# Performance work log

Measured on AMD Instinct MI355X. Metric: run time of the kernel, lower is better.

Reference implementation:

```python
import jax, jax.numpy as jnp
import numpy as np

N = 100000   # nodes
E = 1600000  # edges
D = 128      # input_dim
H = 128      # hidden_dim
O = 64       # output_dim


def setup_inputs() -> dict:
    key = jax.random.key(0)
    ks = jax.random.split(key, 8)
    x = jax.random.normal(ks[0], (N, D), dtype=jnp.float32)
    edge_index = jax.random.randint(ks[1], (2, E), 0, N, dtype=jnp.int32)
    # Glorot-ish init for weights, zeros for biases (matches GCNConv/Linear defaults in spirit)
    W1 = jax.random.normal(ks[2], (D, H), dtype=jnp.float32) / np.sqrt(D)
    b1 = jnp.zeros((H,), dtype=jnp.float32)
    W2 = jax.random.normal(ks[3], (H, H), dtype=jnp.float32) / np.sqrt(H)
    b2 = jnp.zeros((H,), dtype=jnp.float32)
    Wf = jax.random.normal(ks[4], (H, O), dtype=jnp.float32) / np.sqrt(H)
    bf = jnp.zeros((O,), dtype=jnp.float32)
    return {"x": x, "W1": W1, "b1": b1, "W2": W2, "b2": b2,
            "Wf": Wf, "bf": bf, "edge_index": edge_index}


def gcn_conv(x, W, b, src, dst):
    """GCNConv: out = D^{-1/2} (A + I) D^{-1/2} (x W) + b, edges given as (src->dst)."""
    n = x.shape[0]
    h = x @ W  # [N, H]
    loop = jnp.arange(n, dtype=src.dtype)
    s = jnp.concatenate([src, loop])  # add self-loops
    d = jnp.concatenate([dst, loop])
    deg = jax.ops.segment_sum(jnp.ones_like(s, dtype=h.dtype), d, num_segments=n)
    dinv = jnp.where(deg > 0, jax.lax.rsqrt(deg), 0.0)
    coef = dinv[s] * dinv[d]                              # [E+N]
    msg = h[s] * coef[:, None]                            # gather + scale
    out = jax.ops.segment_sum(msg, d, num_segments=n)     # scatter-add aggregate
    return out + b


def reference(x, W1, b1, W2, b2, Wf, bf, edge_index):
    src, dst = edge_index[0], edge_index[1]
    h = jax.nn.relu(gcn_conv(x, W1, b1, src, dst))
    # dropout is identity in eval mode
    h = jax.nn.relu(gcn_conv(h, W2, b2, src, dst))
    return h @ Wf + bf
```

## Files before the change

kernel.cpp:

```cpp
#include <hip/hip_runtime.h>

#define FD 128
#define SCAN_B 256
#define SCAN_T 256


__global__ void k_deg(const int* __restrict__ dst, int* __restrict__ deg, int E) {
  int e = blockIdx.x * blockDim.x + threadIdx.x;
  if (e < E) atomicAdd(&deg[dst[e]], 1);
}


__global__ __launch_bounds__(SCAN_T) void k_part(const int* __restrict__ deg,
                                                 float* __restrict__ dinv,
                                                 int* __restrict__ part, int n) {
  const int b = blockIdx.x;
  const int chunk = (n + SCAN_B - 1) / SCAN_B;
  const int lo = b * chunk;
  const int hi = min(lo + chunk, n);
  int sum = 0;
  for (int i = lo + threadIdx.x; i < hi; i += SCAN_T) {
    int d = deg[i];
    sum += d;
    dinv[i] = rsqrtf((float)(d + 1));
  }
  __shared__ int red[SCAN_T / 64];
  for (int off = 32; off > 0; off >>= 1) sum += __shfl_down(sum, off, 64);
  if ((threadIdx.x & 63) == 0) red[threadIdx.x >> 6] = sum;
  __syncthreads();
  if (threadIdx.x == 0) {
    int s = 0;
#pragma unroll
    for (int w = 0; w < SCAN_T / 64; ++w) s += red[w];
    part[b] = s;
  }
}

__global__ __launch_bounds__(SCAN_B) void k_scanpart(int* __restrict__ part,
                                                     int* __restrict__ row_ptr, int n) {
  __shared__ int s[SCAN_B];
  const int t = threadIdx.x;
  int v = part[t];
  s[t] = v;
  __syncthreads();
  for (int off = 1; off < SCAN_B; off <<= 1) {
    int u = (t >= off) ? s[t - off] : 0;
    __syncthreads();
    s[t] += u;
    __syncthreads();
  }
  part[t] = s[t] - v;
  if (t == SCAN_B - 1) row_ptr[n] = s[t];
}

__global__ __launch_bounds__(SCAN_T) void k_rowptr(const int* __restrict__ deg,
                                                   const int* __restrict__ part,
                                                   int* __restrict__ row_ptr,
                                                   int* __restrict__ cursor, int n) {
  const int b = blockIdx.x;
  const int chunk = (n + SCAN_B - 1) / SCAN_B;
  const int lo = b * chunk;
  const int hi = min(lo + chunk, n);
  const int sub = (chunk + SCAN_T - 1) / SCAN_T;
  const int t = threadIdx.x;
  const int slo = min(lo + t * sub, hi);
  const int shi = min(slo + sub, hi);
  int sum = 0;
  for (int i = slo; i < shi; ++i) sum += deg[i];
  __shared__ int s[SCAN_T];
  s[t] = sum;
  __syncthreads();
  for (int off = 1; off < SCAN_T; off <<= 1) {
    int u = (t >= off) ? s[t - off] : 0;
    __syncthreads();
    s[t] += u;
    __syncthreads();
  }
  int run = part[b] + s[t] - sum;
  for (int i = slo; i < shi; ++i) {
    row_ptr[i] = run;
    cursor[i]  = run;
    run += deg[i];
  }
}


__global__ void k_fill(const int* __restrict__ src, const int* __restrict__ dst,
                       const float* __restrict__ dinv, int* __restrict__ cursor,
                       int2* __restrict__ csr, int E) {
  int e = blockIdx.x * blockDim.x + threadIdx.x;
  if (e < E) {
    int s = src[e], d = dst[e];
    int pos = atomicAdd(&cursor[d], 1);
    csr[pos] = make_int2(s, __float_as_int(dinv[s] * dinv[d]));
  }
}


__global__ __launch_bounds__(256) void k_gemm(const float* __restrict__ A, int lda,
                                              const float* __restrict__ W, int ldw,
                                              const float* __restrict__ bias,
                                              float* __restrict__ out, int ldo, int nrows) {
  __shared__ float Ws[64 * 64];
  __shared__ float xsT[64 * 128];
  const int t  = threadIdx.x;
  const int c0 = blockIdx.y * 64;
  const int r0 = blockIdx.x * 128;

  const int rgrp = t & 31;
  const int cgrp = t >> 5;

  float acc[4][8];
#pragma unroll
  for (int i = 0; i < 4; ++i)
#pragma unroll
    for (int j = 0; j < 8; ++j)
      acc[i][j] = bias ? bias[c0 + cgrp * 8 + j] : 0.f;

  const int rr = t & 127;
  const int hk = t >> 7;

  for (int half = 0; half < 2; ++half) {
    const int kbase = half * 64;
    __syncthreads();
    for (int i = t; i < 64 * 16; i += 256) {
      int k  = i >> 4;
      int c4 = (i & 15) << 2;
      *reinterpret_cast<float4*>(&Ws[k * 64 + c4]) =
          *reinterpret_cast<const float4*>(&W[(size_t)(kbase + k) * ldw + c0 + c4]);
    }
    {
      const int row = r0 + rr;
      const float* ap = &A[(size_t)row * lda + kbase + hk * 32];
#pragma unroll
      for (int j = 0; j < 8; ++j) {
        float4 v = make_float4(0.f, 0.f, 0.f, 0.f);
        if (row < nrows) v = *reinterpret_cast<const float4*>(ap + j * 4);
        const int kb = hk * 32 + j * 4;
        xsT[(kb + 0) * 128 + rr] = v.x;
        xsT[(kb + 1) * 128 + rr] = v.y;
        xsT[(kb + 2) * 128 + rr] = v.z;
        xsT[(kb + 3) * 128 + rr] = v.w;
      }
    }
    __syncthreads();
#pragma unroll 4
    for (int k = 0; k < 64; ++k) {
      const float4 xv = *reinterpret_cast<const float4*>(&xsT[k * 128 + rgrp * 4]);
      const float4 w0 = *reinterpret_cast<const float4*>(&Ws[k * 64 + cgrp * 8]);
      const float4 w1 = *reinterpret_cast<const float4*>(&Ws[k * 64 + cgrp * 8 + 4]);
      const float x[4] = {xv.x, xv.y, xv.z, xv.w};
      const float w[8] = {w0.x, w0.y, w0.z, w0.w, w1.x, w1.y, w1.z, w1.w};
#pragma unroll
      for (int i = 0; i < 4; ++i)
#pragma unroll
        for (int j = 0; j < 8; ++j)
          acc[i][j] += x[i] * w[j];
    }
  }

#pragma unroll
  for (int i = 0; i < 4; ++i) {
    const int row = r0 + rgrp * 4 + i;
    if (row < nrows) {
      float* o = &out[(size_t)row * ldo + c0 + cgrp * 8];
      *reinterpret_cast<float4*>(o)     = make_float4(acc[i][0], acc[i][1], acc[i][2], acc[i][3]);
      *reinterpret_cast<float4*>(o + 4) = make_float4(acc[i][4], acc[i][5], acc[i][6], acc[i][7]);
    }
  }
}


__global__ __launch_bounds__(256) void k_agg(const float* __restrict__ h,
                                             const int* __restrict__ row_ptr,
                                             const int2* __restrict__ csr,
                                             const float* __restrict__ dinv,
                                             const float* __restrict__ bias,
                                             float* __restrict__ out, int n) {
  const int node = blockIdx.x * 4 + (threadIdx.x >> 6);
  if (node >= n) return;
  const int f2 = (threadIdx.x & 63) << 1;
  const float di = dinv[node];
  float2 hv = *reinterpret_cast<const float2*>(&h[(size_t)node * FD + f2]);
  float accx = hv.x * di * di;
  float accy = hv.y * di * di;
  const int e0 = row_ptr[node], e1 = row_ptr[node + 1];
  int e = e0;
  for (; e + 4 <= e1; e += 4) {
    const int2 E0 = csr[e];
    const int2 E1 = csr[e + 1];
    const int2 E2 = csr[e + 2];
    const int2 E3 = csr[e + 3];
    const float2 v0 = *reinterpret_cast<const float2*>(&h[(size_t)E0.x * FD + f2]);
    const float2 v1 = *reinterpret_cast<const float2*>(&h[(size_t)E1.x * FD + f2]);
    const float2 v2 = *reinterpret_cast<const float2*>(&h[(size_t)E2.x * FD + f2]);
    const float2 v3 = *reinterpret_cast<const float2*>(&h[(size_t)E3.x * FD + f2]);
    const float c0 = __int_as_float(E0.y);
    const float c1 = __int_as_float(E1.y);
    const float c2 = __int_as_float(E2.y);
    const float c3 = __int_as_float(E3.y);
    accx += v0.x * c0; accy += v0.y * c0;
    accx += v1.x * c1; accy += v1.y * c1;
    accx += v2.x * c2; accy += v2.y * c2;
    accx += v3.x * c3; accy += v3.y * c3;
  }
  for (; e < e1; ++e) {
    const int2 E0 = csr[e];
    const float c = __int_as_float(E0.y);
    const float2 v = *reinterpret_cast<const float2*>(&h[(size_t)E0.x * FD + f2]);
    accx += v.x * c; accy += v.y * c;
  }
  float2 o;
  o.x = fmaxf(accx + bias[f2],     0.f);
  o.y = fmaxf(accy + bias[f2 + 1], 0.f);
  *reinterpret_cast<float2*>(&out[(size_t)node * FD + f2]) = o;
}


extern "C" void kernel_launch(void* const* d_in, const int* in_sizes, int n_in,
                              void* d_out, int out_size, void* d_ws, size_t ws_size,
                              hipStream_t stream) {
  const float* x  = (const float*)d_in[0];
  const float* W1 = (const float*)d_in[1];
  const float* b1 = (const float*)d_in[2];
  const float* W2 = (const float*)d_in[3];
  const float* b2 = (const float*)d_in[4];
  const float* Wf = (const float*)d_in[5];
  const float* bf = (const float*)d_in[6];
  const int*   ei = (const int*)d_in[7];

  const int N = in_sizes[0] / FD;
  const int E = in_sizes[7] / 2;
  const int O = in_sizes[6];
  const int* src = ei;
  const int* dst = ei + E;

  char* ws = (char*)d_ws;
  size_t off = 0;
  auto alloc = [&](size_t bytes) -> void* {
    void* p = ws + off;
    off += (bytes + 255) & ~(size_t)255;
    return p;
  };
  float* A       = (float*)alloc((size_t)N * FD * 4);
  float* B       = (float*)alloc((size_t)N * FD * 4);
  int*   deg     = (int*)  alloc((size_t)N * 4);
  float* dinv    = (float*)alloc((size_t)N * 4);
  int*   row_ptr = (int*)  alloc((size_t)(N + 1) * 4);
  int*   cursor  = (int*)  alloc((size_t)N * 4);
  int2*  csr     = (int2*) alloc((size_t)E * 8);
  int*   part    = (int*)  alloc((size_t)SCAN_B * 4);

  hipMemsetAsync(deg, 0, (size_t)N * 4, stream);
  k_deg     <<<(E + 255) / 256, 256, 0, stream>>>(dst, deg, E);
  k_part    <<<SCAN_B, SCAN_T, 0, stream>>>(deg, dinv, part, N);
  k_scanpart<<<1, SCAN_B, 0, stream>>>(part, row_ptr, N);
  k_rowptr  <<<SCAN_B, SCAN_T, 0, stream>>>(deg, part, row_ptr, cursor, N);
  k_fill    <<<(E + 255) / 256, 256, 0, stream>>>(src, dst, dinv, cursor, csr, E);

  const int gx = (N + 127) / 128;
  k_gemm<<<dim3(gx, 2), 256, 0, stream>>>(x, FD, W1, FD, nullptr, A, FD, N);
  k_agg <<<(N + 3) / 4, 256, 0, stream>>>(A, row_ptr, csr, dinv, b1, B, N);
  k_gemm<<<dim3(gx, 2), 256, 0, stream>>>(B, FD, W2, FD, nullptr, A, FD, N);
  k_agg <<<(N + 3) / 4, 256, 0, stream>>>(A, row_ptr, csr, dinv, b2, B, N);
  k_gemm<<<dim3(gx, 1), 256, 0, stream>>>(B, FD, Wf, O, bf, (float*)d_out, O, N);
}
```

Before: 643.3 us.

## Store only source ids in CSR and split wavefront across two edges with float4 loads

The CSR array now holds only source indices, and the edge coefficient is recomputed in the aggregation kernel from dinv. This halves CSR storage and the fill kernel's writes, at the cost of an extra dinv gather per edge. The aggregation kernel now has each 64-lane wavefront process two edges at once, with each half-wave loading a float4 slice of a 128-wide row. The two halves are combined with a cross-lane shuffle, which raises memory-level parallelism per wavefront but leaves half the lanes idle on the final store.

```diff
diff --git a/kernel.cpp b/kernel.cpp
--- a/kernel.cpp
+++ b/kernel.cpp
@@ -86,13 +86,12 @@
 
 
 __global__ void k_fill(const int* __restrict__ src, const int* __restrict__ dst,
-                       const float* __restrict__ dinv, int* __restrict__ cursor,
-                       int2* __restrict__ csr, int E) {
+                       int* __restrict__ cursor, int* __restrict__ csr_src, int E) {
   int e = blockIdx.x * blockDim.x + threadIdx.x;
   if (e < E) {
     int s = src[e], d = dst[e];
     int pos = atomicAdd(&cursor[d], 1);
-    csr[pos] = make_int2(s, __float_as_int(dinv[s] * dinv[d]));
+    csr_src[pos] = s;
   }
 }
 
@@ -173,47 +172,65 @@
 
 __global__ __launch_bounds__(256) void k_agg(const float* __restrict__ h,
                                              const int* __restrict__ row_ptr,
-                                             const int2* __restrict__ csr,
+                                             const int* __restrict__ csr_src,
                                              const float* __restrict__ dinv,
                                              const float* __restrict__ bias,
                                              float* __restrict__ out, int n) {
   const int node = blockIdx.x * 4 + (threadIdx.x >> 6);
   if (node >= n) return;
-  const int f2 = (threadIdx.x & 63) << 1;
+  const int lane = threadIdx.x & 63;
+  const int sub  = lane >> 5;
+  const int c4   = (lane & 31) << 2;
   const float di = dinv[node];
-  float2 hv = *reinterpret_cast<const float2*>(&h[(size_t)node * FD + f2]);
-  float accx = hv.x * di * di;
-  float accy = hv.y * di * di;
+
+  float4 acc = make_float4(0.f, 0.f, 0.f, 0.f);
   const int e0 = row_ptr[node], e1 = row_ptr[node + 1];
   int e = e0;
-  for (; e + 4 <= e1; e += 4) {
-    const int2 E0 = csr[e];
-    const int2 E1 = csr[e + 1];
-    const int2 E2 = csr[e + 2];
-    const int2 E3 = csr[e + 3];
-    const float2 v0 = *reinterpret_cast<const float2*>(&h[(size_t)E0.x * FD + f2]);
-    const float2 v1 = *reinterpret_cast<const float2*>(&h[(size_t)E1.x * FD + f2]);
-    const float2 v2 = *reinterpret_cast<const float2*>(&h[(size_t)E2.x * FD + f2]);
-    const float2 v3 = *reinterpret_cast<const float2*>(&h[(size_t)E3.x * FD + f2]);
-    const float c0 = __int_as_float(E0.y);
-    const float c1 = __int_as_float(E1.y);
-    const float c2 = __int_as_float(E2.y);
-    const float c3 = __int_as_float(E3.y);
-    accx += v0.x * c0; accy += v0.y * c0;
-    accx += v1.x * c1; accy += v1.y * c1;
-    accx += v2.x * c2; accy += v2.y * c2;
-    accx += v3.x * c3; accy += v3.y * c3;
-  }
-  for (; e < e1; ++e) {
-    const int2 E0 = csr[e];
-    const float c = __int_as_float(E0.y);
-    const float2 v = *reinterpret_cast<const float2*>(&h[(size_t)E0.x * FD + f2]);
-    accx += v.x * c; accy += v.y * c;
-  }
-  float2 o;
-  o.x = fmaxf(accx + bias[f2],     0.f);
-  o.y = fmaxf(accy + bias[f2 + 1], 0.f);
-  *reinterpret_cast<float2*>(&out[(size_t)node * FD + f2]) = o;
+  for (; e + 8 <= e1; e += 8) {
+    const int ia = csr_src[e     + sub];
+    const int ib = csr_src[e + 2 + sub];
+    const int ic = csr_src[e + 4 + sub];
+    const int id = csr_src[e + 6 + sub];
+    const float4 va = *reinterpret_cast<const float4*>(&h[(size_t)ia * FD + c4]);
+    const float4 vb = *reinterpret_cast<const float4*>(&h[(size_t)ib * FD + c4]);
+    const float4 vc = *reinterpret_cast<const float4*>(&h[(size_t)ic * FD + c4]);
+    const float4 vd = *reinterpret_cast<const float4*>(&h[(size_t)id * FD + c4]);
+    const float ca = dinv[ia] * di;
+    const float cb = dinv[ib] * di;
+    const float cc = dinv[ic] * di;
+    const float cd = dinv[id] * di;
+    acc.x += va.x * ca + vb.x * cb + vc.x * cc + vd.x * cd;
+    acc.y += va.y * ca + vb.y * cb + vc.y * cc + vd.y * cd;
+    acc.z += va.z * ca + vb.z * cb + vc.z * cc + vd.z * cd;
+    acc.w += va.w * ca + vb.w * cb + vc.w * cc + vd.w * cd;
+  }
+  for (; e + 2 <= e1; e += 2) {
+    const int i0 = csr_src[e + sub];
+    const float4 v = *reinterpret_cast<const float4*>(&h[(size_t)i0 * FD + c4]);
+    const float c = dinv[i0] * di;
+    acc.x += v.x * c; acc.y += v.y * c; acc.z += v.z * c; acc.w += v.w * c;
+  }
+  if (e < e1 && sub == 0) {
+    const int i0 = csr_src[e];
+    const float4 v = *reinterpret_cast<const float4*>(&h[(size_t)i0 * FD + c4]);
+    const float c = dinv[i0] * di;
+    acc.x += v.x * c; acc.y += v.y * c; acc.z += v.z * c; acc.w += v.w * c;
+  }
+
+  acc.x += __shfl_xor(acc.x, 32);
+  acc.y += __shfl_xor(acc.y, 32);
+  acc.z += __shfl_xor(acc.z, 32);
+  acc.w += __shfl_xor(acc.w, 32);
+
+  const float4 hs = *reinterpret_cast<const float4*>(&h[(size_t)node * FD + c4]);
+  const float4 b4 = *reinterpret_cast<const float4*>(&bias[c4]);
+  float4 o;
+  o.x = fmaxf(acc.x + hs.x * di * di + b4.x, 0.f);
+  o.y = fmaxf(acc.y + hs.y * di * di + b4.y, 0.f);
+  o.z = fmaxf(acc.z + hs.z * di * di + b4.z, 0.f);
+  o.w = fmaxf(acc.w + hs.w * di * di + b4.w, 0.f);
+  if (sub == 0)
+    *reinterpret_cast<float4*>(&out[(size_t)node * FD + c4]) = o;
 }
 
 
@@ -248,7 +265,7 @@
   float* dinv    = (float*)alloc((size_t)N * 4);
   int*   row_ptr = (int*)  alloc((size_t)(N + 1) * 4);
   int*   cursor  = (int*)  alloc((size_t)N * 4);
-  int2*  csr     = (int2*) alloc((size_t)E * 8);
+  int*   csr_src = (int*)  alloc((size_t)E * 4);
   int*   part    = (int*)  alloc((size_t)SCAN_B * 4);
 
   hipMemsetAsync(deg, 0, (size_t)N * 4, stream);
@@ -256,12 +273,12 @@
   k_part    <<<SCAN_B, SCAN_T, 0, stream>>>(deg, dinv, part, N);
   k_scanpart<<<1, SCAN_B, 0, stream>>>(part, row_ptr, N);
   k_rowptr  <<<SCAN_B, SCAN_T, 0, stream>>>(deg, part, row_ptr, cursor, N);
-  k_fill    <<<(E + 255) / 256, 256, 0, stream>>>(src, dst, dinv, cursor, csr, E);
+  k_fill    <<<(E + 255) / 256, 256, 0, stream>>>(src, dst, cursor, csr_src, E);
 
   const int gx = (N + 127) / 128;
   k_gemm<<<dim3(gx, 2), 256, 0, stream>>>(x, FD, W1, FD, nullptr, A, FD, N);
-  k_agg <<<(N + 3) / 4, 256, 0, stream>>>(A, row_ptr, csr, dinv, b1, B, N);
+  k_agg <<<(N + 3) / 4, 256, 0, stream>>>(A, row_ptr, csr_src, dinv, b1, B, N);
   k_gemm<<<dim3(gx, 2), 256, 0, stream>>>(B, FD, W2, FD, nullptr, A, FD, N);
-  k_agg <<<(N + 3) / 4, 256, 0, stream>>>(A, row_ptr, csr, dinv, b2, B, N);
+  k_agg <<<(N + 3) / 4, 256, 0, stream>>>(A, row_ptr, csr_src, dinv, b2, B, N);
   k_gemm<<<dim3(gx, 1), 256, 0, stream>>>(B, FD, Wf, O, bf, (float*)d_out, O, N);
 }
```

Result: slower. 677.4 us (+5.3%).
